# Performance work log

Measured on AMD Instinct MI355X. Metric: run time of the kernel, lower is better.

## Reference

```python
import jax, jax.numpy as jnp
import numpy as np

# dims: batch, seq(tokens, excl cls), input_dim, embed_dim, heads, ffn, experts, proto experts, classes
B, S, DIN, D, H, FF, E, P, NC = 2, 2048, 1024, 512, 8, 2048, 6, 4, 2
CAP = int(1.0 * S / E)  # capacity_factor=1.0


def _ln(x, g, b, eps=1e-5):
    m = x.mean(-1, keepdims=True)
    v = ((x - m) ** 2).mean(-1, keepdims=True)
    return (x - m) / jnp.sqrt(v + eps) * g + b


def _gelu(x):
    return jax.nn.gelu(x, approximate=False)


def _mha(x, in_w, in_b, out_w, out_b):
    # torch nn.MultiheadAttention, batch_first, eval (no dropout)
    b, s, d = x.shape
    dh = d // H
    qkv = x @ in_w.T + in_b
    q, k, v = jnp.split(qkv, 3, axis=-1)
    q = q.reshape(b, s, H, dh)
    k = k.reshape(b, s, H, dh)
    v = v.reshape(b, s, H, dh)
    att = jnp.einsum('bqhd,bkhd->bhqk', q, k) * (1.0 / np.sqrt(dh))
    att = jax.nn.softmax(att, axis=-1)
    o = jnp.einsum('bhqk,bkhd->bqhd', att, v).reshape(b, s, d)
    return o @ out_w.T + out_b


def _subln_ffn(x, w1, b1, lg, lb, w2, b2):
    # FeedForwardNetwork with subln: fc1 -> gelu -> LayerNorm -> fc2 (eval: no dropout)
    h = _gelu(x @ w1 + b1)
    h = _ln(h, lg, lb)
    return h @ w2 + b2


def _pamoe(x, gate_w, W1, b1, W2, b2):
    # top-1 prototype-augmented MoE with capacity-based token drop
    gate = jax.nn.softmax(x @ gate_w, axis=-1)          # [B,S,E]
    idx = jnp.argmax(gate, axis=-1)                      # [B,S]
    top_p = jnp.max(gate, axis=-1)                       # [B,S]
    oh = jax.nn.one_hot(idx, E, dtype=x.dtype)           # [B,S,E]
    pos = jnp.cumsum(oh, axis=1) * oh                    # position within expert
    keep = oh * (pos <= CAP)                             # capacity mask
    out = jnp.zeros_like(x)
    for e in range(E):  # small fixed loop over experts
        m = (keep[..., e] * top_p)[..., None]
        out = out + m * (_gelu(x @ W1[e] + b1[e]) @ W2[e] + b2[e])
    return out, gate


def _pamoe_ce(gate, labels):
    # CE between renormalized prototype-expert gate probs and cosine-sim labels
    p = gate[..., :P]
    logp = jnp.log(p / p.sum(-1, keepdims=True) + 1e-9)
    nll = -jnp.take_along_axis(logp, labels[..., None], axis=-1)[..., 0]
    return nll.mean()


def setup_inputs() -> dict:
    key = jax.random.key(0)
    cnt = [0]
    def nk():
        cnt[0] += 1
        return jax.random.fold_in(key, cnt[0])
    def w(*shape):
        return jax.random.normal(nk(), shape, dtype=jnp.float32) * 0.02
    d = {}
    d['x'] = jax.random.normal(nk(), (B, S, DIN), dtype=jnp.float32)
    d['protos'] = jax.random.normal(nk(), (P, DIN), dtype=jnp.float32)
    d['cls_token'] = jax.random.normal(nk(), (1, 1, D), dtype=jnp.float32)
    d['fc1_w'] = w(DIN, D); d['fc1_b'] = jnp.zeros((D,), jnp.float32)
    for li in ('l0', 'l1'):
        d[li + '_attn_in_w'] = w(3 * D, D); d[li + '_attn_in_b'] = jnp.zeros((3 * D,), jnp.float32)
        d[li + '_attn_out_w'] = w(D, D); d[li + '_attn_out_b'] = jnp.zeros((D,), jnp.float32)
        d[li + '_n1_g'] = jnp.ones((D,), jnp.float32); d[li + '_n1_b'] = jnp.zeros((D,), jnp.float32)
        d[li + '_n2_g'] = jnp.ones((D,), jnp.float32); d[li + '_n2_b'] = jnp.zeros((D,), jnp.float32)
    # layer0: pamoe + cls_ffn
    d['l0_cls_w1'] = w(D, FF); d['l0_cls_b1'] = jnp.zeros((FF,), jnp.float32)
    d['l0_cls_ln_g'] = jnp.ones((FF,), jnp.float32); d['l0_cls_ln_b'] = jnp.zeros((FF,), jnp.float32)
    d['l0_cls_w2'] = w(FF, D); d['l0_cls_b2'] = jnp.zeros((D,), jnp.float32)
    d['l0_gate_w'] = w(D, E)
    d['l0_e_w1'] = w(E, D, FF); d['l0_e_b1'] = jnp.zeros((E, FF), jnp.float32)
    d['l0_e_w2'] = w(E, FF, D); d['l0_e_b2'] = jnp.zeros((E, D), jnp.float32)
    # layer1: dense ffn
    d['l1_ffn_w1'] = w(D, FF); d['l1_ffn_b1'] = jnp.zeros((FF,), jnp.float32)
    d['l1_ffn_ln_g'] = jnp.ones((FF,), jnp.float32); d['l1_ffn_ln_b'] = jnp.zeros((FF,), jnp.float32)
    d['l1_ffn_w2'] = w(FF, D); d['l1_ffn_b2'] = jnp.zeros((D,), jnp.float32)
    d['norm_g'] = jnp.ones((D,), jnp.float32); d['norm_b'] = jnp.zeros((D,), jnp.float32)
    d['fc2_w'] = w(D, NC); d['fc2_b'] = jnp.zeros((NC,), jnp.float32)
    return d


def reference(x, protos, cls_token, fc1_w, fc1_b,
              l0_attn_in_w, l0_attn_in_b, l0_attn_out_w, l0_attn_out_b,
              l0_n1_g, l0_n1_b, l0_n2_g, l0_n2_b,
              l0_cls_w1, l0_cls_b1, l0_cls_ln_g, l0_cls_ln_b, l0_cls_w2, l0_cls_b2,
              l0_gate_w, l0_e_w1, l0_e_b1, l0_e_w2, l0_e_b2,
              l1_attn_in_w, l1_attn_in_b, l1_attn_out_w, l1_attn_out_b,
              l1_n1_g, l1_n1_b, l1_n2_g, l1_n2_b,
              l1_ffn_w1, l1_ffn_b1, l1_ffn_ln_g, l1_ffn_ln_b, l1_ffn_w2, l1_ffn_b2,
              norm_g, norm_b, fc2_w, fc2_b):
    # prototype cosine similarity on raw (detached) features -> routing supervision labels
    xr = jax.lax.stop_gradient(x)
    xn = xr / (jnp.linalg.norm(xr, axis=-1, keepdims=True) + 1e-8)
    pn = protos / (jnp.linalg.norm(protos, axis=-1, keepdims=True) + 1e-8)
    sim = jnp.einsum('bsd,pd->bsp', xn, pn)             # [B,S,P]
    labels = jnp.argmax(sim, axis=-1)                    # [B,S]

    h = x @ fc1_w + fc1_b                                # [B,S,D]
    cls = jnp.broadcast_to(cls_token, (h.shape[0], 1, D))
    h = jnp.concatenate([cls, h], axis=1)                # [B,S+1,D]

    # ---- layer 0 (pamoe block) ----
    attn = _mha(h, l0_attn_in_w, l0_attn_in_b, l0_attn_out_w, l0_attn_out_b)
    h = _ln(h, l0_n1_g, l0_n1_b)
    h = h + attn
    h = _ln(h, l0_n2_g, l0_n2_b)
    h_res = h
    c = _subln_ffn(h[:, 0:1], l0_cls_w1, l0_cls_b1, l0_cls_ln_g, l0_cls_ln_b, l0_cls_w2, l0_cls_b2)
    t, gate = _pamoe(h[:, 1:], l0_gate_w, l0_e_w1, l0_e_b1, l0_e_w2, l0_e_b2)
    h = h_res + jnp.concatenate([c, t], axis=1)          # pamoe residual
    loss_pamoe = _pamoe_ce(gate, labels)

    # ---- layer 1 (dense ffn block) ----
    attn = _mha(h, l1_attn_in_w, l1_attn_in_b, l1_attn_out_w, l1_attn_out_b)
    h = _ln(h, l1_n1_g, l1_n1_b)
    h = h + attn
    h = _ln(h, l1_n2_g, l1_n2_b)
    h = h + _subln_ffn(h, l1_ffn_w1, l1_ffn_b1, l1_ffn_ln_g, l1_ffn_ln_b, l1_ffn_w2, l1_ffn_b2)

    pooled = _ln(h, norm_g, norm_b)[:, 0]                # cls token
    logits = pooled @ fc2_w + fc2_b                      # [B,NC]
    return gate, logits, loss_pamoe
```

## Files before the change

kernel.cpp:

```cpp
#include <hip/hip_runtime.h>
#include <cmath>

#define DEVINL __device__ __forceinline__

typedef unsigned short ushort_t;
typedef unsigned int uint_t;

constexpr int Bb   = 2;
constexpr int Ss   = 2048;
constexpr int S1   = 2049;
constexpr int DIN  = 1024;
constexpr int Dd   = 512;
constexpr int Hh   = 8;
constexpr int FF   = 2048;
constexpr int Ee   = 6;
constexpr int NCc  = 2;
constexpr int CAP  = 341;
constexpr int NTOK = Bb * Ss;
constexpr int RR   = Bb * S1;
constexpr int MOE_ROWS = Bb * CAP;

typedef __attribute__((ext_vector_type(4))) float f32x4;
typedef __attribute__((ext_vector_type(8))) short bf16x8;

// ... 43 lines not shown

__global__ __launch_bounds__(256) void tpose_cast_kernel(const float* __restrict__ in,
                                                         ushort_t* __restrict__ outp,
                                                         int K, int N) {
  __shared__ float t[64][65];
  const int z = blockIdx.z;
  const float* src = in + (size_t)z * K * N;
  ushort_t* dst = outp + (size_t)z * K * N;
  const int k0 = blockIdx.x * 64, n0 = blockIdx.y * 64;
  const int tx = threadIdx.x & 15, ty = threadIdx.x >> 4;
#pragma unroll
  for (int p = 0; p < 4; ++p) {
    int k = ty + p * 16;
    float4 v = *(const float4*)(src + (size_t)(k0 + k) * N + n0 + tx * 4);
    t[k][tx * 4 + 0] = v.x; t[k][tx * 4 + 1] = v.y;
    t[k][tx * 4 + 2] = v.z; t[k][tx * 4 + 3] = v.w;
  }
  __syncthreads();
#pragma unroll
  for (int p = 0; p < 4; ++p) {
    int n = ty + p * 16;
    uint_t lo = (uint_t)f2bf(t[tx * 4 + 0][n]) | ((uint_t)f2bf(t[tx * 4 + 1][n]) << 16);
    uint_t hi = (uint_t)f2bf(t[tx * 4 + 2][n]) | ((uint_t)f2bf(t[tx * 4 + 3][n]) << 16);
    *(uint2*)(dst + (size_t)(n0 + n) * K + k0 + tx * 4) = make_uint2(lo, hi);
  }
}

__global__ __launch_bounds__(256) void labels_kernel(const float* __restrict__ x,
                                                     const float* __restrict__ protos,
                                                     int* __restrict__ lbl) {
  int t = blockIdx.x * 4 + (threadIdx.x >> 6);
  int lane = threadIdx.x & 63;
  if (t >= NTOK) return;
  const float* xr = x + (size_t)t * DIN;
  float xv[16];
  float ss = 0.f;
#pragma unroll
  for (int i = 0; i < 16; ++i) { xv[i] = xr[lane + 64 * i]; ss += xv[i] * xv[i]; }
  ss = wsum(ss);
  float nx = sqrtf(ss) + 1e-8f;
  float best = -2e30f; int bi = 0;
  for (int p = 0; p < 4; ++p) {
    const float* pr = protos + (size_t)p * DIN;
    float dp = 0.f, pp = 0.f;
#pragma unroll
    for (int i = 0; i < 16; ++i) { float v = pr[lane + 64 * i]; dp += v * xv[i]; pp += v * v; }
    dp = wsum(dp); pp = wsum(pp);
    float sim = dp / (nx * (sqrtf(pp) + 1e-8f));
    if (sim > best) { best = sim; bi = p; }
  }
  if (lane == 0) lbl[t] = bi;
}

template <bool ACT, bool SHIFT>
__global__ __launch_bounds__(256) void mgemm_kernel(const ushort_t* __restrict__ A, int lda,
                                                    const ushort_t* __restrict__ Bw, int ldb,
                                                    const float* __restrict__ bias,
                                                    const ushort_t* __restrict__ res,
                                                    ushort_t* __restrict__ C, int ldc,
                                                    int M, int N, int K) {
  __shared__ ushort_t As[128 * 64];
  __shared__ ushort_t Bs[128 * 64];
  const int tid = threadIdx.x;
  const int l = tid & 63, l15 = l & 15, lg = l >> 4;
  const int w = tid >> 6;
  const int wm = w >> 1, wn = w & 1;
  const int bm = blockIdx.x * 128, bn = blockIdx.y * 128;
  const int srow = w * 32 + (l >> 3);
  const int scc = ((l & 7) ^ (l >> 3)) * 8;

  f32x4 acc[4][4];
#pragma unroll
  for (int i = 0; i < 4; ++i)
#pragma unroll
    for (int j = 0; j < 4; ++j) acc[i][j] = (f32x4){0.f, 0.f, 0.f, 0.f};

  const ushort_t* agp[4];
  const ushort_t* bgp[4];
#pragma unroll
  for (int j = 0; j < 4; ++j) {
    int ar = bm + srow + j * 8; if (ar > M - 1) ar = M - 1;
    agp[j] = A + (size_t)ar * lda + scc;
    bgp[j] = Bw + (size_t)(bn + srow + j * 8) * ldb + scc;
  }

  for (int k0 = 0; k0 < K; k0 += 64) {
#pragma unroll
    for (int j = 0; j < 4; ++j) {
      glds16(agp[j] + k0, (char*)As + w * 4096 + j * 1024);
      glds16(bgp[j] + k0, (char*)Bs + w * 4096 + j * 1024);
    }
    __syncthreads();
#pragma unroll
    for (int kc = 0; kc < 2; ++kc) {
      bf16x8 af[4], bfr[4];
#pragma unroll
      for (int mi = 0; mi < 4; ++mi) {
        int row = wm * 64 + mi * 16 + l15;
        af[mi] = *(const bf16x8*)((const char*)As +
                   ((row * 128 + (kc * 32 + lg * 8) * 2) ^ ((row & 7) << 4)));
      }
#pragma unroll
      for (int ni = 0; ni < 4; ++ni) {
        int row = wn * 64 + ni * 16 + l15;
        bfr[ni] = *(const bf16x8*)((const char*)Bs +
                   ((row * 128 + (kc * 32 + lg * 8) * 2) ^ ((row & 7) << 4)));
      }
#pragma unroll
      for (int mi = 0; mi < 4; ++mi)
#pragma unroll
        for (int ni = 0; ni < 4; ++ni)
          acc[mi][ni] = __builtin_amdgcn_mfma_f32_16x16x32_bf16(af[mi], bfr[ni], acc[mi][ni], 0, 0, 0);
    }
    __syncthreads();
  }

#pragma unroll
  for (int mi = 0; mi < 4; ++mi)
#pragma unroll
    for (int r = 0; r < 4; ++r) {
      int row = bm + wm * 64 + mi * 16 + lg * 4 + r;
      if (row < M) {
        int orow = SHIFT ? (row + (row >> 11) + 1) : row;
#pragma unroll
        for (int ni = 0; ni < 4; ++ni) {
          int col = bn + wn * 64 + ni * 16 + l15;
          float t = acc[mi][ni][r];
          if (bias) t += bias[col];
          if (ACT) t = geluf(t);
          if (res) t += bf2f(res[(size_t)orow * ldc + col]);
          C[(size_t)orow * ldc + col] = f2bf(t);
        }
      }
    }
}

__global__ __launch_bounds__(256) void moe_mgemm1_kernel(const ushort_t* __restrict__ h2,
                                                         const ushort_t* __restrict__ w1T,
                                                         const float* __restrict__ b1all,
                                                         const int* __restrict__ list,
                                                         const int* __restrict__ cnt,
                                                         ushort_t* __restrict__ hid) {
  __shared__ ushort_t As[128 * 64];
  __shared__ ushort_t Bs[128 * 64];
  const int e = blockIdx.z;
  const int c0 = cnt[e * 2 + 0], c1 = cnt[e * 2 + 1];
  const ushort_t* Bw = w1T + (size_t)e * Dd * FF;
  const int tid = threadIdx.x;
  const int l = tid & 63, l15 = l & 15, lg = l >> 4;
  const int w = tid >> 6;
  const int wm = w >> 1, wn = w & 1;
  const int bm = blockIdx.x * 128, bn = blockIdx.y * 128;
  const int srow = w * 32 + (l >> 3);
  const int scc = ((l & 7) ^ (l >> 3)) * 8;

  f32x4 acc[4][4];
#pragma unroll
  for (int i = 0; i < 4; ++i)
#pragma unroll
    for (int j = 0; j < 4; ++j) acc[i][j] = (f32x4){0.f, 0.f, 0.f, 0.f};

  const ushort_t* agp[4];
  const ushort_t* bgp[4];
#pragma unroll
  for (int j = 0; j < 4; ++j) {
    int r = bm + srow + j * 8; if (r > MOE_ROWS - 1) r = MOE_ROWS - 1;
    int tok = list[e * MOE_ROWS + r] & (NTOK - 1);
    int b = tok >> 11, s = tok & (Ss - 1);
    agp[j] = h2 + (size_t)(b * S1 + s + 1) * Dd + scc;
    bgp[j] = Bw + (size_t)(bn + srow + j * 8) * Dd + scc;
  }

  for (int k0 = 0; k0 < Dd; k0 += 64) {
#pragma unroll
    for (int j = 0; j < 4; ++j) {
      glds16(agp[j] + k0, (char*)As + w * 4096 + j * 1024);
      glds16(bgp[j] + k0, (char*)Bs + w * 4096 + j * 1024);
    }
    __syncthreads();
#pragma unroll
    for (int kc = 0; kc < 2; ++kc) {
      bf16x8 af[4], bfr[4];
#pragma unroll
      for (int mi = 0; mi < 4; ++mi) {
        int row = wm * 64 + mi * 16 + l15;
        af[mi] = *(const bf16x8*)((const char*)As +
                   ((row * 128 + (kc * 32 + lg * 8) * 2) ^ ((row & 7) << 4)));
      }
#pragma unroll
      for (int ni = 0; ni < 4; ++ni) {
        int row = wn * 64 + ni * 16 + l15;
        bfr[ni] = *(const bf16x8*)((const char*)Bs +
                   ((row * 128 + (kc * 32 + lg * 8) * 2) ^ ((row & 7) << 4)));
      }
#pragma unroll
      for (int mi = 0; mi < 4; ++mi)
#pragma unroll
        for (int ni = 0; ni < 4; ++ni)
          acc[mi][ni] = __builtin_amdgcn_mfma_f32_16x16x32_bf16(af[mi], bfr[ni], acc[mi][ni], 0, 0, 0);
    }
    __syncthreads();
  }

#pragma unroll
  for (int mi = 0; mi < 4; ++mi)
#pragma unroll
    for (int rr = 0; rr < 4; ++rr) {
      int row = bm + wm * 64 + mi * 16 + lg * 4 + rr;
      bool v2 = (row < MOE_ROWS) && ((row < CAP) ? (row < c0) : ((row - CAP) < c1));
      if (v2) {
#pragma unroll
        for (int ni = 0; ni < 4; ++ni) {
          int col = bn + wn * 64 + ni * 16 + l15;
          hid[((size_t)e * MOE_ROWS + row) * FF + col] =
              f2bf(geluf(acc[mi][ni][rr] + b1all[e * FF + col]));
        }
      }
    }
}

__global__ __launch_bounds__(256) void moe_mgemm2_kernel(const ushort_t* __restrict__ hid,
                                                         const ushort_t* __restrict__ w2T,
                                                         const float* __restrict__ b2all,
                                                         const int* __restrict__ list,
                                                         const int* __restrict__ cnt,
                                                         const float* __restrict__ topp,
                                                         ushort_t* __restrict__ out) {
  __shared__ ushort_t As[128 * 64];
  __shared__ ushort_t Bs[128 * 64];
  const int e = blockIdx.z;
  const int c0 = cnt[e * 2 + 0], c1 = cnt[e * 2 + 1];
  const ushort_t* Bw = w2T + (size_t)e * FF * Dd;
  const int tid = threadIdx.x;
  const int l = tid & 63, l15 = l & 15, lg = l >> 4;
  const int w = tid >> 6;
  const int wm = w >> 1, wn = w & 1;
  const int bm = blockIdx.x * 128, bn = blockIdx.y * 128;
  const int srow = w * 32 + (l >> 3);
  const int scc = ((l & 7) ^ (l >> 3)) * 8;

  f32x4 acc[4][4];
#pragma unroll
  for (int i = 0; i < 4; ++i)
#pragma unroll
    for (int j = 0; j < 4; ++j) acc[i][j] = (f32x4){0.f, 0.f, 0.f, 0.f};

  const ushort_t* agp[4];
  const ushort_t* bgp[4];
#pragma unroll
  for (int j = 0; j < 4; ++j) {
    int r = bm + srow + j * 8; if (r > MOE_ROWS - 1) r = MOE_ROWS - 1;
    agp[j] = hid + ((size_t)e * MOE_ROWS + r) * FF + scc;
    bgp[j] = Bw + (size_t)(bn + srow + j * 8) * FF + scc;
  }

  for (int k0 = 0; k0 < FF; k0 += 64) {
#pragma unroll
    for (int j = 0; j < 4; ++j) {
      glds16(agp[j] + k0, (char*)As + w * 4096 + j * 1024);
      glds16(bgp[j] + k0, (char*)Bs + w * 4096 + j * 1024);
    }
    __syncthreads();
#pragma unroll
    for (int kc = 0; kc < 2; ++kc) {
      bf16x8 af[4], bfr[4];
#pragma unroll
      for (int mi = 0; mi < 4; ++mi) {
        int row = wm * 64 + mi * 16 + l15;
        af[mi] = *(const bf16x8*)((const char*)As +
                   ((row * 128 + (kc * 32 + lg * 8) * 2) ^ ((row & 7) << 4)));
      }
#pragma unroll
      for (int ni = 0; ni < 4; ++ni) {
        int row = wn * 64 + ni * 16 + l15;
        bfr[ni] = *(const bf16x8*)((const char*)Bs +
                   ((row * 128 + (kc * 32 + lg * 8) * 2) ^ ((row & 7) << 4)));
      }
#pragma unroll
      for (int mi = 0; mi < 4; ++mi)
#pragma unroll
        for (int ni = 0; ni < 4; ++ni)
          acc[mi][ni] = __builtin_amdgcn_mfma_f32_16x16x32_bf16(af[mi], bfr[ni], acc[mi][ni], 0, 0, 0);
    }
    __syncthreads();
  }

#pragma unroll
  for (int mi = 0; mi < 4; ++mi)
#pragma unroll
    for (int rr = 0; rr < 4; ++rr) {
      int row = bm + wm * 64 + mi * 16 + lg * 4 + rr;
      bool v2 = (row < MOE_ROWS) && ((row < CAP) ? (row < c0) : ((row - CAP) < c1));
      if (v2) {
        int tok = list[e * MOE_ROWS + row];
        int b = tok >> 11, s = tok & (Ss - 1);
        float tp = topp[tok];
#pragma unroll
        for (int ni = 0; ni < 4; ++ni) {
          int col = bn + wn * 64 + ni * 16 + l15;
          size_t oidx = (size_t)(b * S1 + s + 1) * Dd + col;
          out[oidx] = f2bf(bf2f(out[oidx]) + tp * (acc[mi][ni][rr] + b2all[e * Dd + col]));
        }
      }
    }
}

__global__ __launch_bounds__(256) void cls_fill_kernel(const float* __restrict__ cls,
                                                       ushort_t* __restrict__ h) {
  int i = threadIdx.x;
  uint_t pk = (uint_t)f2bf(cls[i * 2]) | ((uint_t)f2bf(cls[i * 2 + 1]) << 16);
  *(uint_t*)(h + i * 2) = pk;
  *(uint_t*)(h + (size_t)S1 * Dd + i * 2) = pk;
}

template <int EPL>
__global__ __launch_bounds__(256) void ln_wave_kernel(const ushort_t* __restrict__ in,
                                                      const ushort_t* __restrict__ addv,
                                                      const float* __restrict__ g,
                                                      const float* __restrict__ bvec,
                                                      ushort_t* __restrict__ out,
                                                      ushort_t* __restrict__ out2,
                                                      int nrows) {
  constexpr int N = 64 * EPL;
  const int row = blockIdx.x * 4 + (threadIdx.x >> 6);
  const int lane = threadIdx.x & 63;
  if (row >= nrows) return;
  const size_t base = (size_t)row * N + lane * EPL;
  float xf[EPL];
  float s1 = 0.f, s2 = 0.f;
#pragma unroll
  for (int c = 0; c < EPL / 8; ++c) {
    bf16x8 x8 = *(const bf16x8*)(in + base + c * 8);
#pragma unroll
    for (int j = 0; j < 8; ++j) {
      float v = bf2f((ushort_t)x8[j]);
      xf[c * 8 + j] = v;
      s1 += v; s2 += v * v;
    }
  }
  s1 = wsum(s1); s2 = wsum(s2);
  float mean = s1 * (1.0f / N);
  float var = s2 * (1.0f / N) - mean * mean;
  float rstd = rsqrtf(var + 1e-5f);
#pragma unroll
// ... 11 lines not shown
    *(bf16x8*)(out + base + c * 8) = o8;
    if (out2) *(bf16x8*)(out2 + base + c * 8) = o8;
  }
}

__global__ __launch_bounds__(256) void ln2_wave_kernel(const ushort_t* __restrict__ in,
                                                       const ushort_t* __restrict__ addv,
                                                       const float* __restrict__ g1,
                                                       const float* __restrict__ b1,
                                                       const float* __restrict__ g2,
                                                       const float* __restrict__ b2,
                                                       ushort_t* __restrict__ out,
                                                       ushort_t* __restrict__ out2,
                                                       int nrows) {
  constexpr int N = 512;
  const int row = blockIdx.x * 4 + (threadIdx.x >> 6);
  const int lane = threadIdx.x & 63;
  if (row >= nrows) return;
  const size_t base = (size_t)row * N + lane * 8;
  bf16x8 x8 = *(const bf16x8*)(in + base);
  bf16x8 a8 = *(const bf16x8*)(addv + base);
  float xf[8];
  float s1 = 0.f, s2 = 0.f;
#pragma unroll
  for (int j = 0; j < 8; ++j) {
    float v = bf2f((ushort_t)x8[j]);
    xf[j] = v; s1 += v; s2 += v * v;
  }
  s1 = wsum(s1); s2 = wsum(s2);
  float mean = s1 * (1.0f / N);
  float rstd = rsqrtf(s2 * (1.0f / N) - mean * mean + 1e-5f);
  float vf[8];
  float t1 = 0.f, t2 = 0.f;
#pragma unroll
  for (int j = 0; j < 8; ++j) {
    int col = lane * 8 + j;
    float v = (xf[j] - mean) * rstd * g1[col] + b1[col] + bf2f((ushort_t)a8[j]);
    vf[j] = v; t1 += v; t2 += v * v;
  }
  t1 = wsum(t1); t2 = wsum(t2);
  float mean2 = t1 * (1.0f / N);
  float rstd2 = rsqrtf(t2 * (1.0f / N) - mean2 * mean2 + 1e-5f);
  bf16x8 o8;
#pragma unroll
  for (int j = 0; j < 8; ++j) {
    int col = lane * 8 + j;
    o8[j] = (short)f2bf((vf[j] - mean2) * rstd2 * g2[col] + b2[col]);
  }
  *(bf16x8*)(out + base) = o8;
  if (out2) *(bf16x8*)(out2 + base) = o8;
}

__global__ __launch_bounds__(256) void attn_mfma_kernel(const ushort_t* __restrict__ qkv,
                                                        ushort_t* __restrict__ o) {
  __shared__ ushort_t Ksh[64 * 64];
  __shared__ ushort_t Vt[64 * 64];
  const int tid = threadIdx.x;
  const int w = tid >> 6, l = tid & 63;
  const int l15 = l & 15, lg = l >> 4;
  const int hh = blockIdx.y, b = blockIdx.z;
  const int qblk = blockIdx.x * 64;
  const size_t rbase = (size_t)b * S1 * 1536;
  const float CEXP = 0.125f * 1.4426950408889634f;

  bf16x8 aq[2];
  {
    int qr = qblk + w * 16 + l15;
    const ushort_t* qp = qkv + rbase + (size_t)qr * 1536 + hh * 64;
#pragma unroll
    for (int dc = 0; dc < 2; ++dc)
      aq[dc] = (qr < S1) ? *(const bf16x8*)(qp + dc * 32 + lg * 8)
                         : (bf16x8){0, 0, 0, 0, 0, 0, 0, 0};
  }

  f32x4 ovac[4];
#pragma unroll
  for (int dt = 0; dt < 4; ++dt) ovac[dt] = (f32x4){0.f, 0.f, 0.f, 0.f};
  float m_r = -1e30f, l_r = 0.f;

  const int sk_r = tid >> 3, sk_c = tid & 7;
  const int sv_k0 = (tid & 31) * 2, sv_d0 = (tid >> 5) * 8;

  for (int c = 0; c < 33; ++c) {
#pragma unroll
    for (int pass = 0; pass < 2; ++pass) {
      int r = sk_r + pass * 32;
      int key = c * 64 + r;
      bf16x8 v;
      if (key < S1)
        v = *(const bf16x8*)(qkv + rbase + (size_t)key * 1536 + 512 + hh * 64 + sk_c * 8);
      else
        v = (bf16x8){0, 0, 0, 0, 0, 0, 0, 0};
      *(bf16x8*)((char*)Ksh + (((r * 64 + sk_c * 8) * 2) ^ ((r & 7) << 4))) = v;
    }
    {
      int key0 = c * 64 + sv_k0;
      const ushort_t* vp = qkv + rbase + (size_t)key0 * 1536 + 1024 + hh * 64 + sv_d0;
      bf16x8 va, vb;
      if (key0 < S1) va = *(const bf16x8*)(vp);
      else va = (bf16x8){0, 0, 0, 0, 0, 0, 0, 0};
      if (key0 + 1 < S1) vb = *(const bf16x8*)(vp + 1536);
      else vb = (bf16x8){0, 0, 0, 0, 0, 0, 0, 0};
#pragma unroll
      for (int i = 0; i < 8; ++i) {
        uint_t pk = (uint_t)(ushort_t)va[i] | ((uint_t)(ushort_t)vb[i] << 16);
        int d = sv_d0 + i;
        *(uint_t*)((char*)Vt + (((d * 64 + sv_k0) * 2) ^ ((d & 7) << 4))) = pk;
      }
    }
    __syncthreads();

    f32x4 s[4];
    __builtin_amdgcn_s_setprio(1);
#pragma unroll
    for (int kt = 0; kt < 4; ++kt) {
      f32x4 acc = (f32x4){0.f, 0.f, 0.f, 0.f};
      const int krow = kt * 16 + l15;
      const int rswz = (krow & 7) << 4;
#pragma unroll
      for (int dc = 0; dc < 2; ++dc) {
        bf16x8 kb = *(const bf16x8*)((const char*)Ksh + (((krow * 64 + dc * 32 + lg * 8) * 2) ^ rswz));
        acc = __builtin_amdgcn_mfma_f32_16x16x32_bf16(kb, aq[dc], acc, 0, 0, 0);
      }
      s[kt] = acc;
    }
    __builtin_amdgcn_s_setprio(0);
    if (c == 32) {
#pragma unroll
      for (int kt = 0; kt < 4; ++kt)
#pragma unroll
        for (int r = 0; r < 4; ++r)
          if (2048 + kt * 16 + lg * 4 + r >= S1) s[kt][r] = -1e30f;
    }

    f32x4 m4 = (f32x4){fmaxf(s[0][0], s[1][0]), fmaxf(s[0][1], s[1][1]),
                       fmaxf(s[0][2], s[1][2]), fmaxf(s[0][3], s[1][3])};
#pragma unroll
    for (int r = 0; r < 4; ++r) m4[r] = fmaxf(m4[r], fmaxf(s[2][r], s[3][r]));
    float mx = fmaxf(fmaxf(m4[0], m4[1]), fmaxf(m4[2], m4[3]));
    mx = fmaxf(mx, __shfl_xor(mx, 16));
    mx = fmaxf(mx, __shfl_xor(mx, 32));
    float mn = fmaxf(m_r, mx);
    float fac = __builtin_amdgcn_exp2f((m_r - mn) * CEXP);
    m_r = mn;
    float mc = mn * CEXP;
    float p[4][4];
    float rs = 0.f;
#pragma unroll
    for (int kt = 0; kt < 4; ++kt)
#pragma unroll
      for (int r = 0; r < 4; ++r) {
        float pv = __builtin_amdgcn_exp2f(s[kt][r] * CEXP - mc);
        p[kt][r] = pv;
        rs += pv;
      }
    rs += __shfl_xor(rs, 16);
    rs += __shfl_xor(rs, 32);
    l_r = l_r * fac + rs;

    uint_t pk[4][2];
#pragma unroll
    for (int kt = 0; kt < 4; ++kt) {
      pk[kt][0] = (uint_t)f2bf(p[kt][0]) | ((uint_t)f2bf(p[kt][1]) << 16);
      pk[kt][1] = (uint_t)f2bf(p[kt][2]) | ((uint_t)f2bf(p[kt][3]) << 16);
    }

    float facq[4];
#pragma unroll
    for (int r = 0; r < 4; ++r) facq[r] = __shfl(fac, lg * 4 + r);
#pragma unroll
    for (int dt = 0; dt < 4; ++dt)
#pragma unroll
      for (int r = 0; r < 4; ++r) ovac[dt][r] *= facq[r];

    bf16x8 pa[2];
#pragma unroll
    for (int kh = 0; kh < 2; ++kh) {
      union { uint_t u[4]; bf16x8 v; } cu;
#pragma unroll
      for (int wd = 0; wd < 4; ++wd) {
        int src = (((2 * lg + (wd >> 1)) & 3) << 4) + l15;
        uint_t c0 = (uint_t)__shfl((int)pk[kh * 2 + 0][wd & 1], src);
        uint_t c1 = (uint_t)__shfl((int)pk[kh * 2 + 1][wd & 1], src);
        cu.u[wd] = (lg & 2) ? c1 : c0;
      }
      pa[kh] = cu.v;
    }

    __builtin_amdgcn_s_setprio(1);
#pragma unroll
    for (int kh = 0; kh < 2; ++kh)
#pragma unroll
      for (int dt = 0; dt < 4; ++dt) {
        const int vrow = dt * 16 + l15;
        bf16x8 vb = *(const bf16x8*)((const char*)Vt +
                      (((vrow * 64 + kh * 32 + lg * 8) * 2) ^ ((vrow & 7) << 4)));
        ovac[dt] = __builtin_amdgcn_mfma_f32_16x16x32_bf16(pa[kh], vb, ovac[dt], 0, 0, 0);
      }
    __builtin_amdgcn_s_setprio(0);
    __syncthreads();
  }

  float invq[4];
#pragma unroll
  for (int r = 0; r < 4; ++r) invq[r] = 1.0f / __shfl(l_r, lg * 4 + r);
#pragma unroll
  for (int r = 0; r < 4; ++r) {
    int qq = qblk + w * 16 + lg * 4 + r;
    if (qq < S1) {
      ushort_t* orow = o + (size_t)(b * S1 + qq) * Dd + hh * 64;
#pragma unroll
      for (int dt = 0; dt < 4; ++dt) orow[dt * 16 + l15] = f2bf(ovac[dt][r] * invq[r]);
    }
  }
}

__global__ __launch_bounds__(256) void gate_kernel(const ushort_t* __restrict__ h2,
                                                   const float* __restrict__ gw,
                                                   float* __restrict__ gate_out,
                                                   float* __restrict__ topp,
                                                   int* __restrict__ idx) {
  int t = blockIdx.x * 4 + (threadIdx.x >> 6);
  int lane = threadIdx.x & 63;
  if (t >= NTOK) return;
  int b = t >> 11, s = t & (Ss - 1);
  const ushort_t* hr = h2 + (size_t)(b * S1 + s + 1) * Dd;
  bf16x8 h8 = *(const bf16x8*)(hr + lane * 8);
  float acc[6] = {};
#pragma unroll
  for (int j = 0; j < 8; ++j) {
    int d = lane * 8 + j;
    float xv = bf2f((ushort_t)h8[j]);
    const float* g = gw + (size_t)d * Ee;
#pragma unroll
    for (int e = 0; e < 6; ++e) acc[e] += xv * g[e];
  }
#pragma unroll
  for (int e = 0; e < 6; ++e) acc[e] = wsum(acc[e]);
  if (lane == 0) {
    float mx = acc[0];
#pragma unroll
    for (int e = 1; e < 6; ++e) mx = fmaxf(mx, acc[e]);
    float ex[6], sum = 0.f;
#pragma unroll
    for (int e = 0; e < 6; ++e) { ex[e] = __expf(acc[e] - mx); sum += ex[e]; }
    float invs = 1.0f / sum;
    int best = 0; float bp = ex[0];
#pragma unroll
    for (int e = 1; e < 6; ++e) { if (ex[e] > bp) { bp = ex[e]; best = e; } }
#pragma unroll
    for (int e = 0; e < 6; ++e) gate_out[(size_t)t * Ee + e] = ex[e] * invs;
    topp[t] = bp * invs;
    idx[t] = best;
  }
}

__global__ __launch_bounds__(256) void route_kernel(const int* __restrict__ idx,
                                                    int* __restrict__ list,
                                                    int* __restrict__ cnt) {
  __shared__ int cnts[256];
  __shared__ int tot;
  const int e = blockIdx.x, b = blockIdx.y;
  const int tid = threadIdx.x;
  const int s0 = tid * 8;
  int loc[8];
  int c = 0;
#pragma unroll
// ... 167 lines not shown
  const float* n2b0    = (const float*)d_in[12];
  const float* a1_in_w = (const float*)d_in[13];
  const float* a1_in_b = (const float*)d_in[14];
  const float* a1_out_w= (const float*)d_in[15];
  const float* a1_out_b= (const float*)d_in[16];
  const float* n1g1    = (const float*)d_in[17];
  const float* n1b1    = (const float*)d_in[18];
  const float* n2g1    = (const float*)d_in[19];
  const float* n2b1    = (const float*)d_in[20];
  const float* cw1     = (const float*)d_in[21];
  const float* cb1     = (const float*)d_in[22];
  const float* clg     = (const float*)d_in[23];
  const float* clb     = (const float*)d_in[24];
  const float* cw2     = (const float*)d_in[25];
  const float* cb2     = (const float*)d_in[26];
  const float* gate_w  = (const float*)d_in[27];
  const float* ew1     = (const float*)d_in[28];
  const float* eb1     = (const float*)d_in[29];
  const float* ew2     = (const float*)d_in[30];
  const float* eb2     = (const float*)d_in[31];
  const float* fw1     = (const float*)d_in[32];
  const float* fb1     = (const float*)d_in[33];
  const float* flg     = (const float*)d_in[34];
  const float* flb     = (const float*)d_in[35];
  const float* fw2     = (const float*)d_in[36];
  const float* fb2     = (const float*)d_in[37];
  const float* ng      = (const float*)d_in[38];
  const float* nb      = (const float*)d_in[39];
  const float* fc2_w   = (const float*)d_in[40];
  const float* fc2_b   = (const float*)d_in[41];
  float* out = (float*)d_out;

  char* base = (char*)d_ws;
  size_t o = 0;
  auto alloc = [&](size_t bytes) -> void* {
    void* p = base + o;
    o += (bytes + 255) & ~(size_t)255;
    return p;
  };
  ushort_t* UB0  = (ushort_t*)alloc((size_t)RR * Dd * 2);
  ushort_t* UB1  = (ushort_t*)alloc((size_t)RR * Dd * 2);
  ushort_t* UB2  = (ushort_t*)alloc((size_t)RR * Dd * 2);
  ushort_t* BIGU = (ushort_t*)alloc((size_t)RR * FF * 2);
  ushort_t* XB   = (ushort_t*)alloc((size_t)NTOK * DIN * 2);
  ushort_t* WQ0  = (ushort_t*)alloc((size_t)3 * Dd * Dd * 2);
  ushort_t* WO0  = (ushort_t*)alloc((size_t)Dd * Dd * 2);
  ushort_t* WQ1  = (ushort_t*)alloc((size_t)3 * Dd * Dd * 2);
  ushort_t* WO1  = (ushort_t*)alloc((size_t)Dd * Dd * 2);
  ushort_t* WF1T = (ushort_t*)alloc((size_t)Dd * DIN * 2);
  ushort_t* WE1T = (ushort_t*)alloc((size_t)Ee * FF * Dd * 2);
  ushort_t* WE2T = (ushort_t*)alloc((size_t)Ee * Dd * FF * 2);
  ushort_t* WFW1T= (ushort_t*)alloc((size_t)FF * Dd * 2);
  ushort_t* WFW2T= (ushort_t*)alloc((size_t)Dd * FF * 2);
  float* TOPP = (float*)alloc(NTOK * 4);
  float* PART = (float*)alloc(64 * 4);
  float* CHID = (float*)alloc(Bb * FF * 4);
  float* CHLN = (float*)alloc(Bb * FF * 4);
  int* LBL  = (int*)alloc(NTOK * 4);
  int* IDX  = (int*)alloc(NTOK * 4);
  int* LIST = (int*)alloc(Ee * MOE_ROWS * 4);
  int* CNT  = (int*)alloc(Ee * Bb * 4);

  const int ln_grid = (RR + 3) / 4;

  cast_kernel<<<(NTOK * DIN / 8 + 255) / 256, 256, 0, stream>>>(x, XB, NTOK * DIN / 8);
  cast_kernel<<<(3 * Dd * Dd / 8 + 255) / 256, 256, 0, stream>>>(a0_in_w, WQ0, 3 * Dd * Dd / 8);
  cast_kernel<<<(Dd * Dd / 8 + 255) / 256, 256, 0, stream>>>(a0_out_w, WO0, Dd * Dd / 8);
  cast_kernel<<<(3 * Dd * Dd / 8 + 255) / 256, 256, 0, stream>>>(a1_in_w, WQ1, 3 * Dd * Dd / 8);
  cast_kernel<<<(Dd * Dd / 8 + 255) / 256, 256, 0, stream>>>(a1_out_w, WO1, Dd * Dd / 8);
  tpose_cast_kernel<<<dim3(DIN / 64, Dd / 64, 1), 256, 0, stream>>>(fc1_w, WF1T, DIN, Dd);
  tpose_cast_kernel<<<dim3(Dd / 64, FF / 64, Ee), 256, 0, stream>>>(ew1, WE1T, Dd, FF);
  tpose_cast_kernel<<<dim3(FF / 64, Dd / 64, Ee), 256, 0, stream>>>(ew2, WE2T, FF, Dd);
  tpose_cast_kernel<<<dim3(Dd / 64, FF / 64, 1), 256, 0, stream>>>(fw1, WFW1T, Dd, FF);
  tpose_cast_kernel<<<dim3(FF / 64, Dd / 64, 1), 256, 0, stream>>>(fw2, WFW2T, FF, Dd);

  labels_kernel<<<NTOK / 4, 256, 0, stream>>>(x, protos, LBL);
  mgemm_kernel<false, true><<<dim3(32, 4), 256, 0, stream>>>(
      XB, DIN, WF1T, DIN, fc1_b, nullptr, UB0, Dd, NTOK, Dd, DIN);
  cls_fill_kernel<<<1, 256, 0, stream>>>(cls_tok, UB0);

  mgemm_kernel<false, false><<<dim3(33, 12), 256, 0, stream>>>(
      UB0, Dd, WQ0, Dd, a0_in_b, nullptr, BIGU, 3 * Dd, RR, 3 * Dd, Dd);
  attn_mfma_kernel<<<dim3(33, Hh, Bb), 256, 0, stream>>>(BIGU, UB1);
  mgemm_kernel<false, false><<<dim3(33, 4), 256, 0, stream>>>(
      UB1, Dd, WO0, Dd, a0_out_b, nullptr, UB2, Dd, RR, Dd, Dd);
  ln2_wave_kernel<<<ln_grid, 256, 0, stream>>>(UB0, UB2, n1g0, n1b0, n2g0, n2b0, UB0, UB2, RR);

  cls_ffn1_kernel<<<dim3(FF / 32, Bb), 256, 0, stream>>>(UB0, cw1, cb1, CHID);
  cls_ln_kernel<<<Bb, 256, 0, stream>>>(CHID, clg, clb, CHLN);
  cls_ffn2_kernel<<<dim3(Dd / 32, Bb), 256, 0, stream>>>(CHLN, cw2, cb2, UB2);
  gate_kernel<<<NTOK / 4, 256, 0, stream>>>(UB0, gate_w, out, TOPP, IDX);
  route_kernel<<<dim3(Ee, Bb), 256, 0, stream>>>(IDX, LIST, CNT);
  moe_mgemm1_kernel<<<dim3(6, 16, Ee), 256, 0, stream>>>(UB0, WE1T, eb1, LIST, CNT, BIGU);
  moe_mgemm2_kernel<<<dim3(6, 4, Ee), 256, 0, stream>>>(BIGU, WE2T, eb2, LIST, CNT, TOPP, UB2);
  loss_part_kernel<<<16, 256, 0, stream>>>(out, LBL, PART);
  loss_final_kernel<<<1, 64, 0, stream>>>(PART, out);

  mgemm_kernel<false, false><<<dim3(33, 12), 256, 0, stream>>>(
      UB2, Dd, WQ1, Dd, a1_in_b, nullptr, BIGU, 3 * Dd, RR, 3 * Dd, Dd);
  attn_mfma_kernel<<<dim3(33, Hh, Bb), 256, 0, stream>>>(BIGU, UB1);
  mgemm_kernel<false, false><<<dim3(33, 4), 256, 0, stream>>>(
      UB1, Dd, WO1, Dd, a1_out_b, nullptr, UB0, Dd, RR, Dd, Dd);
  ln2_wave_kernel<<<ln_grid, 256, 0, stream>>>(UB2, UB0, n1g1, n1b1, n2g1, n2b1, UB2, nullptr, RR);

  mgemm_kernel<true, false><<<dim3(33, 16), 256, 0, stream>>>(
      UB2, Dd, WFW1T, Dd, fb1, nullptr, BIGU, FF, RR, FF, Dd);
  ln_wave_kernel<32><<<ln_grid, 256, 0, stream>>>(BIGU, nullptr, flg, flb, BIGU, nullptr, RR);
  mgemm_kernel<false, false><<<dim3(33, 4), 256, 0, stream>>>(
      BIGU, FF, WFW2T, FF, fb2, UB2, UB0, Dd, RR, Dd, FF);

  final_head_kernel<<<Bb, 256, 0, stream>>>(UB0, ng, nb, fc2_w, fc2_b, out);
}
```

Measured before the change: 572.2 us.

## Split attention over two KV halves with a separate combine kernel

Attention blocks now process only half of the key/value chunks each, doubling the grid, and write unnormalized fp32 partial outputs plus per-row max and sum. A new combine kernel rescales and merges the two halves into the bf16 output. This targets low occupancy and long serial loops on a grid smaller than the device can fill, at the cost of extra fp32 memory traffic and an additional launch per attention layer.

```diff
diff --git a/kernel.cpp b/kernel.cpp
--- a/kernel.cpp
+++ b/kernel.cpp
@@ -474,16 +474,20 @@
 }
 
 __global__ __launch_bounds__(256) void attn_mfma_kernel(const ushort_t* __restrict__ qkv,
-                                                        ushort_t* __restrict__ o) {
+                                                        float* __restrict__ po,
+                                                        float2* __restrict__ ml) {
   __shared__ ushort_t Ksh[64 * 64];
   __shared__ ushort_t Vt[64 * 64];
   const int tid = threadIdx.x;
   const int w = tid >> 6, l = tid & 63;
   const int l15 = l & 15, lg = l >> 4;
-  const int hh = blockIdx.y, b = blockIdx.z;
+  const int hh = blockIdx.y;
+  const int b = blockIdx.z >> 1, kvh = blockIdx.z & 1;
   const int qblk = blockIdx.x * 64;
   const size_t rbase = (size_t)b * S1 * 1536;
   const float CEXP = 0.125f * 1.4426950408889634f;
+  const int cbeg = kvh * 17;
+  const int cend = (kvh == 0) ? 17 : 33;
 
   bf16x8 aq[2];
   {
@@ -503,7 +507,7 @@
   const int sk_r = tid >> 3, sk_c = tid & 7;
   const int sv_k0 = (tid & 31) * 2, sv_d0 = (tid >> 5) * 8;
 
-  for (int c = 0; c < 33; ++c) {
+  for (int c = cbeg; c < cend; ++c) {
 #pragma unroll
     for (int pass = 0; pass < 2; ++pass) {
       int r = sk_r + pass * 32;
@@ -623,18 +627,53 @@
     __syncthreads();
   }
 
-  float invq[4];
-#pragma unroll
-  for (int r = 0; r < 4; ++r) invq[r] = 1.0f / __shfl(l_r, lg * 4 + r);
+  if (lg == 0) {
+    int qq = qblk + w * 16 + l15;
+    if (qq < S1)
+      ml[(((size_t)kvh * Bb + b) * Hh + hh) * S1 + qq] = make_float2(m_r, l_r);
+  }
 #pragma unroll
   for (int r = 0; r < 4; ++r) {
     int qq = qblk + w * 16 + lg * 4 + r;
     if (qq < S1) {
-      ushort_t* orow = o + (size_t)(b * S1 + qq) * Dd + hh * 64;
-#pragma unroll
-      for (int dt = 0; dt < 4; ++dt) orow[dt * 16 + l15] = f2bf(ovac[dt][r] * invq[r]);
-    }
-  }
+      float* orow = po + (((size_t)kvh * Bb + b) * S1 + qq) * Dd + hh * 64;
+#pragma unroll
+      for (int dt = 0; dt < 4; ++dt) orow[dt * 16 + l15] = ovac[dt][r];
+    }
+  }
+}
+
+__global__ __launch_bounds__(256) void attn_combine_kernel(const float* __restrict__ po,
+                                                           const float2* __restrict__ ml,
+                                                           ushort_t* __restrict__ o) {
+  int i = blockIdx.x * 256 + threadIdx.x;
+  if (i >= RR * Dd / 8) return;
+  int qrow = i >> 6;
+  int d8 = (i & 63) * 8;
+  int b = (qrow >= S1) ? 1 : 0;
+  int q = qrow - b * S1;
+  int hh = d8 >> 6;
+  const float CEXP = 0.125f * 1.4426950408889634f;
+  float2 v0 = ml[(((size_t)0 * Bb + b) * Hh + hh) * S1 + q];
+  float2 v1 = ml[(((size_t)1 * Bb + b) * Hh + hh) * S1 + q];
+  float M = fmaxf(v0.x, v1.x);
+  float f0 = exp2f((v0.x - M) * CEXP);
+  float f1 = exp2f((v1.x - M) * CEXP);
+  float inv = 1.0f / (v0.y * f0 + v1.y * f1);
+  const float* p0 = po + ((size_t)b * S1 + q) * Dd + d8;
+  const float* p1 = po + ((size_t)(Bb + b) * S1 + q) * Dd + d8;
+  float4 a0 = *(const float4*)(p0), a1 = *(const float4*)(p0 + 4);
+  float4 c0 = *(const float4*)(p1), c1 = *(const float4*)(p1 + 4);
+  bf16x8 o8;
+  o8[0] = (short)f2bf((a0.x * f0 + c0.x * f1) * inv);
+  o8[1] = (short)f2bf((a0.y * f0 + c0.y * f1) * inv);
+  o8[2] = (short)f2bf((a0.z * f0 + c0.z * f1) * inv);
+  o8[3] = (short)f2bf((a0.w * f0 + c0.w * f1) * inv);
+  o8[4] = (short)f2bf((a1.x * f0 + c1.x * f1) * inv);
+  o8[5] = (short)f2bf((a1.y * f0 + c1.y * f1) * inv);
+  o8[6] = (short)f2bf((a1.z * f0 + c1.z * f1) * inv);
+  o8[7] = (short)f2bf((a1.w * f0 + c1.w * f1) * inv);
+  *(bf16x8*)(o + (size_t)qrow * Dd + d8) = o8;
 }
 
 __global__ __launch_bounds__(256) void gate_kernel(const ushort_t* __restrict__ h2,
@@ -908,6 +947,8 @@
   ushort_t* WE2T = (ushort_t*)alloc((size_t)Ee * Dd * FF * 2);
   ushort_t* WFW1T= (ushort_t*)alloc((size_t)FF * Dd * 2);
   ushort_t* WFW2T= (ushort_t*)alloc((size_t)Dd * FF * 2);
+  float*    PO   = (float*)alloc((size_t)2 * RR * Dd * 4);
+  float2*   ML   = (float2*)alloc((size_t)2 * Bb * Hh * S1 * 8);
   float* TOPP = (float*)alloc(NTOK * 4);
   float* PART = (float*)alloc(64 * 4);
   float* CHID = (float*)alloc(Bb * FF * 4);
@@ -918,6 +959,7 @@
   int* CNT  = (int*)alloc(Ee * Bb * 4);
 
   const int ln_grid = (RR + 3) / 4;
+  const int cmb_grid = (RR * Dd / 8 + 255) / 256;
 
   cast_kernel<<<(NTOK * DIN / 8 + 255) / 256, 256, 0, stream>>>(x, XB, NTOK * DIN / 8);
   cast_kernel<<<(3 * Dd * Dd / 8 + 255) / 256, 256, 0, stream>>>(a0_in_w, WQ0, 3 * Dd * Dd / 8);
@@ -937,7 +979,8 @@
 
   mgemm_kernel<false, false><<<dim3(33, 12), 256, 0, stream>>>(
       UB0, Dd, WQ0, Dd, a0_in_b, nullptr, BIGU, 3 * Dd, RR, 3 * Dd, Dd);
-  attn_mfma_kernel<<<dim3(33, Hh, Bb), 256, 0, stream>>>(BIGU, UB1);
+  attn_mfma_kernel<<<dim3(33, Hh, Bb * 2), 256, 0, stream>>>(BIGU, PO, ML);
+  attn_combine_kernel<<<cmb_grid, 256, 0, stream>>>(PO, ML, UB1);
   mgemm_kernel<false, false><<<dim3(33, 4), 256, 0, stream>>>(
       UB1, Dd, WO0, Dd, a0_out_b, nullptr, UB2, Dd, RR, Dd, Dd);
   ln2_wave_kernel<<<ln_grid, 256, 0, stream>>>(UB0, UB2, n1g0, n1b0, n2g0, n2b0, UB0, UB2, RR);
@@ -954,7 +997,8 @@
 
   mgemm_kernel<false, false><<<dim3(33, 12), 256, 0, stream>>>(
       UB2, Dd, WQ1, Dd, a1_in_b, nullptr, BIGU, 3 * Dd, RR, 3 * Dd, Dd);
-  attn_mfma_kernel<<<dim3(33, Hh, Bb), 256, 0, stream>>>(BIGU, UB1);
+  attn_mfma_kernel<<<dim3(33, Hh, Bb * 2), 256, 0, stream>>>(BIGU, PO, ML);
+  attn_combine_kernel<<<cmb_grid, 256, 0, stream>>>(PO, ML, UB1);
   mgemm_kernel<false, false><<<dim3(33, 4), 256, 0, stream>>>(
       UB1, Dd, WO1, Dd, a1_out_b, nullptr, UB0, Dd, RR, Dd, Dd);
   ln2_wave_kernel<<<ln_grid, 256, 0, stream>>>(UB2, UB0, n1g1, n1b1, n2g1, n2b1, UB2, nullptr, RR);
```

Result: slower. 589.4 us (+3.0%).

## Templatize GEMM M-tile to 64 rows for small-N GEMMs; add lazy softmax rescale

Applied to the files above, without the earlier changes.

The GEMM and MoE second-stage kernels get a template parameter for the M tile height. Most small-N projections and the MoE down-projection now use 64-row tiles, which doubles the grid so more CUs are busy on the 256-CU part. Separately, the flash-attention loop skips the running-max update and accumulator rescale unless the new max exceeds the old by more than a threshold, saving shuffles and multiplies per KV tile. The trade-offs are less operand reuse per block, and the lazy rescale lets exponentials grow up to 2^8 times larger, which could affect accuracy in bf16.

```diff
diff --git a/kernel.cpp b/kernel.cpp
--- a/kernel.cpp
+++ b/kernel.cpp
@@ -119,51 +119,56 @@
   if (lane == 0) lbl[t] = bi;
 }
 
-template <bool ACT, bool SHIFT>
+template <bool ACT, bool SHIFT, int BMT>
 __global__ __launch_bounds__(256) void mgemm_kernel(const ushort_t* __restrict__ A, int lda,
                                                     const ushort_t* __restrict__ Bw, int ldb,
                                                     const float* __restrict__ bias,
                                                     const ushort_t* __restrict__ res,
                                                     ushort_t* __restrict__ C, int ldc,
                                                     int M, int N, int K) {
-  __shared__ ushort_t As[128 * 64];
+  constexpr int MI = BMT / 32;
+  __shared__ ushort_t As[BMT * 64];
   __shared__ ushort_t Bs[128 * 64];
   const int tid = threadIdx.x;
   const int l = tid & 63, l15 = l & 15, lg = l >> 4;
   const int w = tid >> 6;
   const int wm = w >> 1, wn = w & 1;
-  const int bm = blockIdx.x * 128, bn = blockIdx.y * 128;
-  const int srow = w * 32 + (l >> 3);
+  const int bm = blockIdx.x * BMT, bn = blockIdx.y * 128;
+  const int srowA = w * (BMT / 4) + (l >> 3);
+  const int srowB = w * 32 + (l >> 3);
   const int scc = ((l & 7) ^ (l >> 3)) * 8;
 
-  f32x4 acc[4][4];
-#pragma unroll
-  for (int i = 0; i < 4; ++i)
+  f32x4 acc[MI][4];
+#pragma unroll
+  for (int i = 0; i < MI; ++i)
 #pragma unroll
     for (int j = 0; j < 4; ++j) acc[i][j] = (f32x4){0.f, 0.f, 0.f, 0.f};
 
-  const ushort_t* agp[4];
+  const ushort_t* agp[MI];
   const ushort_t* bgp[4];
 #pragma unroll
-  for (int j = 0; j < 4; ++j) {
-    int ar = bm + srow + j * 8; if (ar > M - 1) ar = M - 1;
+  for (int j = 0; j < MI; ++j) {
+    int ar = bm + srowA + j * 8; if (ar > M - 1) ar = M - 1;
     agp[j] = A + (size_t)ar * lda + scc;
-    bgp[j] = Bw + (size_t)(bn + srow + j * 8) * ldb + scc;
-  }
+  }
+#pragma unroll
+  for (int j = 0; j < 4; ++j)
+    bgp[j] = Bw + (size_t)(bn + srowB + j * 8) * ldb + scc;
 
   for (int k0 = 0; k0 < K; k0 += 64) {
 #pragma unroll
-    for (int j = 0; j < 4; ++j) {
-      glds16(agp[j] + k0, (char*)As + w * 4096 + j * 1024);
+    for (int j = 0; j < MI; ++j)
+      glds16(agp[j] + k0, (char*)As + w * (BMT * 32) + j * 1024);
+#pragma unroll
+    for (int j = 0; j < 4; ++j)
       glds16(bgp[j] + k0, (char*)Bs + w * 4096 + j * 1024);
-    }
     __syncthreads();
 #pragma unroll
     for (int kc = 0; kc < 2; ++kc) {
-      bf16x8 af[4], bfr[4];
-#pragma unroll
-      for (int mi = 0; mi < 4; ++mi) {
-        int row = wm * 64 + mi * 16 + l15;
+      bf16x8 af[MI], bfr[4];
+#pragma unroll
+      for (int mi = 0; mi < MI; ++mi) {
+        int row = wm * (BMT / 2) + mi * 16 + l15;
         af[mi] = *(const bf16x8*)((const char*)As +
                    ((row * 128 + (kc * 32 + lg * 8) * 2) ^ ((row & 7) << 4)));
       }
@@ -174,7 +179,7 @@
                    ((row * 128 + (kc * 32 + lg * 8) * 2) ^ ((row & 7) << 4)));
       }
 #pragma unroll
-      for (int mi = 0; mi < 4; ++mi)
+      for (int mi = 0; mi < MI; ++mi)
 #pragma unroll
         for (int ni = 0; ni < 4; ++ni)
           acc[mi][ni] = __builtin_amdgcn_mfma_f32_16x16x32_bf16(af[mi], bfr[ni], acc[mi][ni], 0, 0, 0);
@@ -183,10 +188,10 @@
   }
 
 #pragma unroll
-  for (int mi = 0; mi < 4; ++mi)
+  for (int mi = 0; mi < MI; ++mi)
 #pragma unroll
     for (int r = 0; r < 4; ++r) {
-      int row = bm + wm * 64 + mi * 16 + lg * 4 + r;
+      int row = bm + wm * (BMT / 2) + mi * 16 + lg * 4 + r;
       if (row < M) {
         int orow = SHIFT ? (row + (row >> 11) + 1) : row;
 #pragma unroll
@@ -286,6 +291,7 @@
     }
 }
 
+template <int BMT>
 __global__ __launch_bounds__(256) void moe_mgemm2_kernel(const ushort_t* __restrict__ hid,
                                                          const ushort_t* __restrict__ w2T,
                                                          const float* __restrict__ b2all,
@@ -293,7 +299,8 @@
                                                          const int* __restrict__ cnt,
                                                          const float* __restrict__ topp,
                                                          ushort_t* __restrict__ out) {
-  __shared__ ushort_t As[128 * 64];
+  constexpr int MI = BMT / 32;
+  __shared__ ushort_t As[BMT * 64];
   __shared__ ushort_t Bs[128 * 64];
   const int e = blockIdx.z;
   const int c0 = cnt[e * 2 + 0], c1 = cnt[e * 2 + 1];
@@ -302,38 +309,42 @@
   const int l = tid & 63, l15 = l & 15, lg = l >> 4;
   const int w = tid >> 6;
   const int wm = w >> 1, wn = w & 1;
-  const int bm = blockIdx.x * 128, bn = blockIdx.y * 128;
-  const int srow = w * 32 + (l >> 3);
+  const int bm = blockIdx.x * BMT, bn = blockIdx.y * 128;
+  const int srowA = w * (BMT / 4) + (l >> 3);
+  const int srowB = w * 32 + (l >> 3);
   const int scc = ((l & 7) ^ (l >> 3)) * 8;
 
-  f32x4 acc[4][4];
-#pragma unroll
-  for (int i = 0; i < 4; ++i)
+  f32x4 acc[MI][4];
+#pragma unroll
+  for (int i = 0; i < MI; ++i)
 #pragma unroll
     for (int j = 0; j < 4; ++j) acc[i][j] = (f32x4){0.f, 0.f, 0.f, 0.f};
 
-  const ushort_t* agp[4];
+  const ushort_t* agp[MI];
   const ushort_t* bgp[4];
 #pragma unroll
-  for (int j = 0; j < 4; ++j) {
-    int r = bm + srow + j * 8; if (r > MOE_ROWS - 1) r = MOE_ROWS - 1;
+  for (int j = 0; j < MI; ++j) {
+    int r = bm + srowA + j * 8; if (r > MOE_ROWS - 1) r = MOE_ROWS - 1;
     agp[j] = hid + ((size_t)e * MOE_ROWS + r) * FF + scc;
-    bgp[j] = Bw + (size_t)(bn + srow + j * 8) * FF + scc;
-  }
+  }
+#pragma unroll
+  for (int j = 0; j < 4; ++j)
+    bgp[j] = Bw + (size_t)(bn + srowB + j * 8) * FF + scc;
 
   for (int k0 = 0; k0 < FF; k0 += 64) {
 #pragma unroll
-    for (int j = 0; j < 4; ++j) {
-      glds16(agp[j] + k0, (char*)As + w * 4096 + j * 1024);
+    for (int j = 0; j < MI; ++j)
+      glds16(agp[j] + k0, (char*)As + w * (BMT * 32) + j * 1024);
+#pragma unroll
+    for (int j = 0; j < 4; ++j)
       glds16(bgp[j] + k0, (char*)Bs + w * 4096 + j * 1024);
-    }
     __syncthreads();
 #pragma unroll
     for (int kc = 0; kc < 2; ++kc) {
-      bf16x8 af[4], bfr[4];
-#pragma unroll
-      for (int mi = 0; mi < 4; ++mi) {
-        int row = wm * 64 + mi * 16 + l15;
+      bf16x8 af[MI], bfr[4];
+#pragma unroll
+      for (int mi = 0; mi < MI; ++mi) {
+        int row = wm * (BMT / 2) + mi * 16 + l15;
         af[mi] = *(const bf16x8*)((const char*)As +
                    ((row * 128 + (kc * 32 + lg * 8) * 2) ^ ((row & 7) << 4)));
       }
@@ -344,7 +355,7 @@
                    ((row * 128 + (kc * 32 + lg * 8) * 2) ^ ((row & 7) << 4)));
       }
 #pragma unroll
-      for (int mi = 0; mi < 4; ++mi)
+      for (int mi = 0; mi < MI; ++mi)
 #pragma unroll
         for (int ni = 0; ni < 4; ++ni)
           acc[mi][ni] = __builtin_amdgcn_mfma_f32_16x16x32_bf16(af[mi], bfr[ni], acc[mi][ni], 0, 0, 0);
@@ -353,10 +364,10 @@
   }
 
 #pragma unroll
-  for (int mi = 0; mi < 4; ++mi)
+  for (int mi = 0; mi < MI; ++mi)
 #pragma unroll
     for (int rr = 0; rr < 4; ++rr) {
-      int row = bm + wm * 64 + mi * 16 + lg * 4 + rr;
+      int row = bm + wm * (BMT / 2) + mi * 16 + lg * 4 + rr;
       bool v2 = (row < MOE_ROWS) && ((row < CAP) ? (row < c0) : ((row - CAP) < c1));
       if (v2) {
         int tok = list[e * MOE_ROWS + row];
@@ -562,10 +573,20 @@
     float mx = fmaxf(fmaxf(m4[0], m4[1]), fmaxf(m4[2], m4[3]));
     mx = fmaxf(mx, __shfl_xor(mx, 16));
     mx = fmaxf(mx, __shfl_xor(mx, 32));
-    float mn = fmaxf(m_r, mx);
-    float fac = __builtin_amdgcn_exp2f((m_r - mn) * CEXP);
-    m_r = mn;
-    float mc = mn * CEXP;
+    if (!__all(mx <= m_r + 8.0f)) {
+      float mn = fmaxf(m_r, mx);
+      float fac = __builtin_amdgcn_exp2f((m_r - mn) * CEXP);
+      m_r = mn;
+      float facq[4];
+#pragma unroll
+      for (int r = 0; r < 4; ++r) facq[r] = __shfl(fac, lg * 4 + r);
+#pragma unroll
+      for (int dt = 0; dt < 4; ++dt)
+#pragma unroll
+        for (int r = 0; r < 4; ++r) ovac[dt][r] *= facq[r];
+      l_r *= fac;
+    }
+    float mc = m_r * CEXP;
     float p[4][4];
     float rs = 0.f;
 #pragma unroll
@@ -578,7 +599,7 @@
       }
     rs += __shfl_xor(rs, 16);
     rs += __shfl_xor(rs, 32);
-    l_r = l_r * fac + rs;
+    l_r += rs;
 
     uint_t pk[4][2];
 #pragma unroll
@@ -586,14 +607,6 @@
       pk[kt][0] = (uint_t)f2bf(p[kt][0]) | ((uint_t)f2bf(p[kt][1]) << 16);
       pk[kt][1] = (uint_t)f2bf(p[kt][2]) | ((uint_t)f2bf(p[kt][3]) << 16);
     }
-
-    float facq[4];
-#pragma unroll
-    for (int r = 0; r < 4; ++r) facq[r] = __shfl(fac, lg * 4 + r);
-#pragma unroll
-    for (int dt = 0; dt < 4; ++dt)
-#pragma unroll
-      for (int r = 0; r < 4; ++r) ovac[dt][r] *= facq[r];
 
     bf16x8 pa[2];
 #pragma unroll
@@ -931,14 +944,14 @@
   tpose_cast_kernel<<<dim3(FF / 64, Dd / 64, 1), 256, 0, stream>>>(fw2, WFW2T, FF, Dd);
 
   labels_kernel<<<NTOK / 4, 256, 0, stream>>>(x, protos, LBL);
-  mgemm_kernel<false, true><<<dim3(32, 4), 256, 0, stream>>>(
+  mgemm_kernel<false, true, 64><<<dim3(64, 4), 256, 0, stream>>>(
       XB, DIN, WF1T, DIN, fc1_b, nullptr, UB0, Dd, NTOK, Dd, DIN);
   cls_fill_kernel<<<1, 256, 0, stream>>>(cls_tok, UB0);
 
-  mgemm_kernel<false, false><<<dim3(33, 12), 256, 0, stream>>>(
+  mgemm_kernel<false, false, 64><<<dim3(65, 12), 256, 0, stream>>>(
       UB0, Dd, WQ0, Dd, a0_in_b, nullptr, BIGU, 3 * Dd, RR, 3 * Dd, Dd);
   attn_mfma_kernel<<<dim3(33, Hh, Bb), 256, 0, stream>>>(BIGU, UB1);
-  mgemm_kernel<false, false><<<dim3(33, 4), 256, 0, stream>>>(
+  mgemm_kernel<false, false, 64><<<dim3(65, 4), 256, 0, stream>>>(
       UB1, Dd, WO0, Dd, a0_out_b, nullptr, UB2, Dd, RR, Dd, Dd);
   ln2_wave_kernel<<<ln_grid, 256, 0, stream>>>(UB0, UB2, n1g0, n1b0, n2g0, n2b0, UB0, UB2, RR);
 
@@ -948,21 +961,21 @@
   gate_kernel<<<NTOK / 4, 256, 0, stream>>>(UB0, gate_w, out, TOPP, IDX);
   route_kernel<<<dim3(Ee, Bb), 256, 0, stream>>>(IDX, LIST, CNT);
   moe_mgemm1_kernel<<<dim3(6, 16, Ee), 256, 0, stream>>>(UB0, WE1T, eb1, LIST, CNT, BIGU);
-  moe_mgemm2_kernel<<<dim3(6, 4, Ee), 256, 0, stream>>>(BIGU, WE2T, eb2, LIST, CNT, TOPP, UB2);
+  moe_mgemm2_kernel<64><<<dim3(11, 4, Ee), 256, 0, stream>>>(BIGU, WE2T, eb2, LIST, CNT, TOPP, UB2);
   loss_part_kernel<<<16, 256, 0, stream>>>(out, LBL, PART);
   loss_final_kernel<<<1, 64, 0, stream>>>(PART, out);
 
-  mgemm_kernel<false, false><<<dim3(33, 12), 256, 0, stream>>>(
+  mgemm_kernel<false, false, 64><<<dim3(65, 12), 256, 0, stream>>>(
       UB2, Dd, WQ1, Dd, a1_in_b, nullptr, BIGU, 3 * Dd, RR, 3 * Dd, Dd);
   attn_mfma_kernel<<<dim3(33, Hh, Bb), 256, 0, stream>>>(BIGU, UB1);
-  mgemm_kernel<false, false><<<dim3(33, 4), 256, 0, stream>>>(
+  mgemm_kernel<false, false, 64><<<dim3(65, 4), 256, 0, stream>>>(
       UB1, Dd, WO1, Dd, a1_out_b, nullptr, UB0, Dd, RR, Dd, Dd);
   ln2_wave_kernel<<<ln_grid, 256, 0, stream>>>(UB2, UB0, n1g1, n1b1, n2g1, n2b1, UB2, nullptr, RR);
 
-  mgemm_kernel<true, false><<<dim3(33, 16), 256, 0, stream>>>(
+  mgemm_kernel<true, false, 128><<<dim3(33, 16), 256, 0, stream>>>(
       UB2, Dd, WFW1T, Dd, fb1, nullptr, BIGU, FF, RR, FF, Dd);
   ln_wave_kernel<32><<<ln_grid, 256, 0, stream>>>(BIGU, nullptr, flg, flb, BIGU, nullptr, RR);
-  mgemm_kernel<false, false><<<dim3(33, 4), 256, 0, stream>>>(
+  mgemm_kernel<false, false, 64><<<dim3(65, 4), 256, 0, stream>>>(
       BIGU, FF, WFW2T, FF, fb2, UB2, UB0, Dd, RR, Dd, FF);
 
   final_head_kernel<<<Bb, 256, 0, stream>>>(UB0, ng, nb, fc2_w, fc2_b, out);
```

New measurement: 498.5 us. 12.9% less time.
